# Performance work log

Measured on AMD Instinct MI355X. Metric: run time of the kernel, lower is better.

## Reference

```python
import jax, jax.numpy as jnp
import numpy as np

N_NODES = 50000
N_EDGES = 800000
D = 128  # node_dim == edge_dim
NEG_SLOPE = 0.2


def setup_inputs() -> dict:
    key = jax.random.key(0)
    ks = jax.random.split(key, 16)
    w = lambda k, shp: (jax.random.normal(k, shp, dtype=jnp.float32) * 0.02)
    b = lambda: jnp.zeros((D,), dtype=jnp.float32)
    return {
        "V": jax.random.normal(ks[0], (N_NODES, D), dtype=jnp.float32),
        "E": jax.random.normal(ks[1], (N_EDGES, D), dtype=jnp.float32),
        "src": jax.random.randint(ks[2], (N_EDGES,), 0, N_NODES, dtype=jnp.int32),
        "dst": jax.random.randint(ks[3], (N_EDGES,), 0, N_NODES, dtype=jnp.int32),
        # NodePooling: two node_dim->node_dim linears
        "Wp1": w(ks[4], (D, D)), "bp1": b(),
        "Wp2": w(ks[5], (D, D)), "bp2": b(),
        # GenMessage.A: MLP with nb_mlp_layer=2 linears (edge_dim->edge_dim)
        "WA1": w(ks[6], (D, D)), "bA1": b(),
        "WA2": w(ks[7], (D, D)), "bA2": b(),
        # GenMessage.B (scale) and .C (shift): edge_dim->node_dim
        "WB": w(ks[8], (D, D)), "bB": b(),
        "WC": w(ks[9], (D, D)), "bC": b(),
    }


def reference(V, E, src, dst, Wp1, bp1, Wp2, bp2, WA1, bA1, WA2, bA2, WB, bB, WC, bC):
    lrelu = lambda x: jax.nn.leaky_relu(x, NEG_SLOPE)
    # V = act(V); G.ndata['V'] = pooling(V)
    Vp = lrelu(lrelu(V) @ Wp1.T + bp1) @ Wp2.T + bp2  # [N, D]
    # edge MLP on edge features (ReLU between linears, none after last)
    x = jax.nn.relu(E @ WA1.T + bA1) @ WA2.T + bA2    # [E, D]
    scale = jax.nn.sigmoid(x @ WB.T + bB)             # [E, D]
    shift = x @ WC.T + bC                             # [E, D]
    # per-edge gated message using gathered source node features
    msg = scale * Vp[src] + shift                     # [E, D]
    # scatter-sum into destination nodes (dgl.fn.sum)
    out = jax.ops.segment_sum(msg, dst, num_segments=N_NODES)  # [N, D]
    return out
```

## Files before the change

kernel.cpp:

```cpp
#include <hip/hip_runtime.h>
#include <hip/hip_bf16.h>

typedef __attribute__((ext_vector_type(8))) short bf16x8;
typedef __attribute__((ext_vector_type(4))) float f32x4;

#define DD 128

static __device__ __forceinline__ unsigned short f2bf(float f) {
    __bf16 h = (__bf16)f;
    return __builtin_bit_cast(unsigned short, h);
}
static __device__ __forceinline__ unsigned int pk2bf(float lo, float hi) {
    return ((unsigned int)f2bf(hi) << 16) | (unsigned int)f2bf(lo);
}
static __device__ __forceinline__ float bf2f(unsigned short h) {
    unsigned int u = ((unsigned int)h) << 16;
    return __builtin_bit_cast(float, u);
}

static __device__ __forceinline__ void lds_barrier() {
    asm volatile("s_waitcnt lgkmcnt(0)" ::: "memory");
    __builtin_amdgcn_s_barrier();
    asm volatile("" ::: "memory");
}

__global__ __launch_bounds__(256) void k_convert_hist(
    const float* __restrict__ w0, const float* __restrict__ w1,
    const float* __restrict__ w2, const float* __restrict__ w3,
    const float* __restrict__ w4, const float* __restrict__ w5,
    unsigned short* __restrict__ wbf,
    const int* __restrict__ dst, int* __restrict__ counts, int nE, int use_perm) {
    int i = blockIdx.x * blockDim.x + threadIdx.x;
    if (i < 6 * 16384) {
        int m = i >> 14, k = i & 16383;
        const float* s = (m == 0) ? w0 : (m == 1) ? w1 : (m == 2) ? w2 : (m == 3) ? w3
                         : (m == 4) ? w4 : w5;
        wbf[i] = f2bf(s[k]);
    }
    if (use_perm)
        for (int e = i; e < nE; e += gridDim.x * blockDim.x)
            atomicAdd(&counts[dst[e]], 1);
}

__global__ __launch_bounds__(256) void k_scanA(const int* __restrict__ counts,
                                               int* __restrict__ cursor,
                                               int* __restrict__ partials, int nN) {
    __shared__ int ps[256];
    const int tid = threadIdx.x;
    const int i = blockIdx.x * 256 + tid;
    int v = (i < nN) ? counts[i] : 0;
    ps[tid] = v;
    __syncthreads();
    for (int off = 1; off < 256; off <<= 1) {
        int add = (tid >= off) ? ps[tid - off] : 0;
        __syncthreads();
        ps[tid] += add;
        __syncthreads();
    }
    if (i < nN) cursor[i] = ps[tid] - v;
    if (tid == 255) partials[blockIdx.x] = ps[255];
}

__global__ __launch_bounds__(256) void k_scanB(int* __restrict__ cursor,
                                               const int* __restrict__ partials,
                                               int nN, int nB) {
    __shared__ int ps[256];
    const int tid = threadIdx.x;
    int v = 0;
    for (int j = tid; j < blockIdx.x; j += 256) v += partials[j];
    ps[tid] = v;
    __syncthreads();
    for (int off = 1; off < 256; off <<= 1) {
        int add = (tid >= off) ? ps[tid - off] : 0;
        __syncthreads();
        ps[tid] += add;
        __syncthreads();
    }
    const int offset = ps[255];
    const int i = blockIdx.x * 256 + tid;
    if (i < nN) cursor[i] += offset;
}

__global__ __launch_bounds__(256, 3) void k_nodes(
    const float* __restrict__ V, const unsigned short* __restrict__ wbf,
    const float* __restrict__ bp1, const float* __restrict__ bp2,
    unsigned short* __restrict__ Vp, int nN, int nTiles,
    const int* __restrict__ dst, int* __restrict__ cursor,
    int* __restrict__ perm, int nE, int use_perm)
{
    if (use_perm)
        for (int e = blockIdx.x * blockDim.x + threadIdx.x; e < nE; e += gridDim.x * blockDim.x) {
            int pos = atomicAdd(&cursor[dst[e]], 1);
            perm[pos] = e;
        }

    const int lane = threadIdx.x & 63;
    const int wave = threadIdx.x >> 6;
    const int lr = lane & 15, lg = lane >> 4;

    bf16x8 B1[2][4], B2[2][4];
#pragma unroll
    for (int ct = 0; ct < 2; ++ct)
#pragma unroll
        for (int kk = 0; kk < 4; ++kk) {
            int j = wave * 32 + ct * 16 + lr;
            int k0 = kk * 32 + lg * 8;
            B1[ct][kk] = *(const bf16x8*)(wbf + 0 * 16384 + j * DD + k0);
            B2[ct][kk] = *(const bf16x8*)(wbf + 1 * 16384 + j * DD + k0);
        }
    float b1v[2], b2v[2];
#pragma unroll
    for (int ct = 0; ct < 2; ++ct) {
        int c = wave * 32 + ct * 16 + lr;
        b1v[ct] = bp1[c]; b2v[ct] = bp2[c];
    }
    __shared__ alignas(16) unsigned short xb[32][136];

    for (int t = blockIdx.x; t < nTiles; t += gridDim.x) {
        const int r0 = t * 32;
        bf16x8 A[2][4];
#pragma unroll
        for (int rg = 0; rg < 2; ++rg)
#pragma unroll
            for (int kk = 0; kk < 4; ++kk) {
                int row = r0 + rg * 16 + lr; if (row >= nN) row = nN - 1;
                const float4* p = (const float4*)(V + (size_t)row * DD + kk * 32 + lg * 8);
                float4 f0 = p[0], f1 = p[1];
                float v[8] = {f0.x, f0.y, f0.z, f0.w, f1.x, f1.y, f1.z, f1.w};
                bf16x8 a;
#pragma unroll
                for (int e = 0; e < 8; ++e) {
                    float x = v[e];
                    x = x > 0.f ? x : 0.2f * x;
                    a[e] = (short)f2bf(x);
                }
                A[rg][kk] = a;
            }
#pragma unroll
        for (int rg = 0; rg < 2; ++rg)
#pragma unroll
            for (int ct = 0; ct < 2; ++ct) {
                f32x4 acc = {0.f, 0.f, 0.f, 0.f};
#pragma unroll
                for (int kk = 0; kk < 4; ++kk)
                    acc = __builtin_amdgcn_mfma_f32_16x16x32_bf16(A[rg][kk], B1[ct][kk], acc, 0, 0, 0);
#pragma unroll
                for (int r = 0; r < 4; ++r) {
                    float x = acc[r] + b1v[ct];
                    x = x > 0.f ? x : 0.2f * x;
                    xb[rg * 16 + lg * 4 + r][wave * 32 + ct * 16 + lr] = f2bf(x);
                }
            }
        lds_barrier();
        bf16x8 A2[2][4];
#pragma unroll
        for (int rg = 0; rg < 2; ++rg)
#pragma unroll
            for (int kk = 0; kk < 4; ++kk)
                A2[rg][kk] = *(const bf16x8*)&xb[rg * 16 + lr][kk * 32 + lg * 8];
#pragma unroll
        for (int rg = 0; rg < 2; ++rg)
#pragma unroll
            for (int ct = 0; ct < 2; ++ct) {
                f32x4 acc = {0.f, 0.f, 0.f, 0.f};
#pragma unroll
                for (int kk = 0; kk < 4; ++kk)
                    acc = __builtin_amdgcn_mfma_f32_16x16x32_bf16(A2[rg][kk], B2[ct][kk], acc, 0, 0, 0);
#pragma unroll
                for (int r = 0; r < 4; ++r) {
                    int row = r0 + rg * 16 + lg * 4 + r;
                    if (row < nN)
                        Vp[(size_t)row * DD + wave * 32 + ct * 16 + lr] = f2bf(acc[r] + b2v[ct]);
                }
            }
        lds_barrier();
    }
}

__global__ __launch_bounds__(256, 2) void k_edges(
    const float* __restrict__ E, const int* __restrict__ src, const int* __restrict__ dst,
    const int* __restrict__ perm, int use_perm,
    const unsigned short* __restrict__ wbf,
    const float* __restrict__ bA1, const float* __restrict__ bA2,
    const float* __restrict__ bB, const float* __restrict__ bC,
    const unsigned short* __restrict__ Vp, float* __restrict__ out, int nE, int nTiles)
{
    const int lane = threadIdx.x & 63;
    const int wave = threadIdx.x >> 6;
    const int lr = lane & 15, lg = lane >> 4;
    const int srow = threadIdx.x >> 3;
    const int schunk = threadIdx.x & 7;

    bf16x8 B1[2][4], B2[2][4], B3[2][4], B4[2][4];
#pragma unroll
    for (int ct = 0; ct < 2; ++ct)
#pragma unroll
        for (int kk = 0; kk < 4; ++kk) {
            int j = wave * 32 + ct * 16 + lr;
            int k0 = kk * 32 + lg * 8;
            const unsigned short* p = wbf + 2 * 16384 + j * DD + k0;
            B1[ct][kk] = *(const bf16x8*)(p);
            B2[ct][kk] = *(const bf16x8*)(p + 16384);
            B3[ct][kk] = *(const bf16x8*)(p + 32768);
            B4[ct][kk] = *(const bf16x8*)(p + 49152);
        }
    float b1v[2], b2v[2], b3v[2], b4v[2];
#pragma unroll
    for (int ct = 0; ct < 2; ++ct) {
        int c = wave * 32 + ct * 16 + lr;
        b1v[ct] = bA1[c]; b2v[ct] = bA2[c]; b3v[ct] = bB[c]; b4v[ct] = bC[c];
    }
    __shared__ alignas(16) unsigned short xb[2][32][136];
    __shared__ alignas(16) unsigned short Eb[2][32][136];
    __shared__ alignas(8)  unsigned short gv[32][132];
    __shared__ int dstb[32];

    const int gstep = gridDim.x;
    int t = blockIdx.x;

    auto pidx = [&](int i) -> int {
        if (i >= nE) i = nE - 1;
        return use_perm ? perm[i] : i;
    };

    int pe_t = pidx(t * 32 + srow);
    int pe1  = pidx((t + gstep) * 32 + srow);
    uint2 g0, g1, g2, g3;
    {
        const uint2* vp2 = (const uint2*)(Vp + (size_t)src[pe_t] * DD);
        g0 = vp2[schunk]; g1 = vp2[schunk + 8]; g2 = vp2[schunk + 16]; g3 = vp2[schunk + 24];
    }
    int pd = ((t * 32 + srow) < nE) ? dst[pe_t] : -1;
    float4 pf0, pf1, pf2, pf3;
    {
        const float4* np = (const float4*)(E + (size_t)pe1 * DD + schunk * 16);
        pf0 = np[0]; pf1 = np[1]; pf2 = np[2]; pf3 = np[3];
    }
    {
        const float4* p = (const float4*)(E + (size_t)pe_t * DD + schunk * 16);
        float4 f0 = p[0], f1 = p[1], f2 = p[2], f3 = p[3];
        uint4 w0 = make_uint4(pk2bf(f0.x, f0.y), pk2bf(f0.z, f0.w),
                              pk2bf(f1.x, f1.y), pk2bf(f1.z, f1.w));
        uint4 w1 = make_uint4(pk2bf(f2.x, f2.y), pk2bf(f2.z, f2.w),
                              pk2bf(f3.x, f3.y), pk2bf(f3.z, f3.w));
        uint4* wp = (uint4*)&Eb[0][srow][schunk * 16];
        wp[0] = w0; wp[1] = w1;
    }
    lds_barrier();
    int cur = 0;

    for (; t < nTiles; t += gstep) {
        bf16x8 A[2][4];
#pragma unroll
        for (int rg = 0; rg < 2; ++rg)
#pragma unroll
            for (int kk = 0; kk < 4; ++kk)
                A[rg][kk] = *(const bf16x8*)&Eb[cur][rg * 16 + lr][kk * 32 + lg * 8];
#pragma unroll
        for (int rg = 0; rg < 2; ++rg)
#pragma unroll
            for (int ct = 0; ct < 2; ++ct) {
                f32x4 acc = {0.f, 0.f, 0.f, 0.f};
#pragma unroll
                for (int kk = 0; kk < 4; ++kk)
                    acc = __builtin_amdgcn_mfma_f32_16x16x32_bf16(A[rg][kk], B1[ct][kk], acc, 0, 0, 0);
#pragma unroll
                for (int r = 0; r < 4; ++r) {
                    float x = fmaxf(acc[r] + b1v[ct], 0.f);
                    xb[0][rg * 16 + lg * 4 + r][wave * 32 + ct * 16 + lr] = f2bf(x);
                }
            }
        lds_barrier();
        *(uint2*)&gv[srow][schunk * 4]      = g0;
        *(uint2*)&gv[srow][schunk * 4 + 32] = g1;
        *(uint2*)&gv[srow][schunk * 4 + 64] = g2;
        *(uint2*)&gv[srow][schunk * 4 + 96] = g3;
        if (schunk == 0) dstb[srow] = pd;
        {
            uint4 w0 = make_uint4(pk2bf(pf0.x, pf0.y), pk2bf(pf0.z, pf0.w),
                                  pk2bf(pf1.x, pf1.y), pk2bf(pf1.z, pf1.w));
            uint4 w1 = make_uint4(pk2bf(pf2.x, pf2.y), pk2bf(pf2.z, pf2.w),
                                  pk2bf(pf3.x, pf3.y), pk2bf(pf3.z, pf3.w));
            uint4* wp = (uint4*)&Eb[cur ^ 1][srow][schunk * 16];
            wp[0] = w0; wp[1] = w1;
        }
        int pe2 = pidx((t + 2 * gstep) * 32 + srow);
        float4 nf0, nf1, nf2, nf3;
        {
            const float4* np = (const float4*)(E + (size_t)pe2 * DD + schunk * 16);
            nf0 = np[0]; nf1 = np[1]; nf2 = np[2]; nf3 = np[3];
        }
        {
            int sl = src[pe1];
            const uint2* nvp2 = (const uint2*)(Vp + (size_t)sl * DD);
            g0 = nvp2[schunk]; g1 = nvp2[schunk + 8]; g2 = nvp2[schunk + 16]; g3 = nvp2[schunk + 24];
        }
        int pdn = (((t + gstep) * 32 + srow) < nE) ? dst[pe1] : -1;
        bf16x8 A2[2][4];
#pragma unroll
        for (int rg = 0; rg < 2; ++rg)
#pragma unroll
            for (int kk = 0; kk < 4; ++kk)
                A2[rg][kk] = *(const bf16x8*)&xb[0][rg * 16 + lr][kk * 32 + lg * 8];
#pragma unroll
        for (int rg = 0; rg < 2; ++rg)
#pragma unroll
            for (int ct = 0; ct < 2; ++ct) {
                f32x4 acc = {0.f, 0.f, 0.f, 0.f};
#pragma unroll
                for (int kk = 0; kk < 4; ++kk)
                    acc = __builtin_amdgcn_mfma_f32_16x16x32_bf16(A2[rg][kk], B2[ct][kk], acc, 0, 0, 0);
#pragma unroll
                for (int r = 0; r < 4; ++r)
                    xb[1][rg * 16 + lg * 4 + r][wave * 32 + ct * 16 + lr] = f2bf(acc[r] + b2v[ct]);
            }
        lds_barrier();
        bf16x8 A3[2][4];
#pragma unroll
        for (int rg = 0; rg < 2; ++rg)
#pragma unroll
            for (int kk = 0; kk < 4; ++kk)
                A3[rg][kk] = *(const bf16x8*)&xb[1][rg * 16 + lr][kk * 32 + lg * 8];
        float mA0[4], mA1[4], mB0[4], mB1[4];
#pragma unroll
        for (int rg = 0; rg < 2; ++rg)
#pragma unroll
            for (int ct = 0; ct < 2; ++ct) {
                f32x4 aB = {0.f, 0.f, 0.f, 0.f}, aC = {0.f, 0.f, 0.f, 0.f};
#pragma unroll
                for (int kk = 0; kk < 4; ++kk) {
                    aB = __builtin_amdgcn_mfma_f32_16x16x32_bf16(A3[rg][kk], B3[ct][kk], aB, 0, 0, 0);
                    aC = __builtin_amdgcn_mfma_f32_16x16x32_bf16(A3[rg][kk], B4[ct][kk], aC, 0, 0, 0);
                }
                const int col = wave * 32 + ct * 16 + lr;
#pragma unroll
                for (int r = 0; r < 4; ++r) {
                    float e = __expf(-(aB[r] + b3v[ct]));
                    float sc = __builtin_amdgcn_rcpf(1.f + e);
                    float sh = aC[r] + b4v[ct];
                    float v = bf2f(gv[rg * 16 + lg * 4 + r][col]);
                    float m = sc * v + sh;
                    if (rg == 0) { if (ct == 0) mA0[r] = m; else mA1[r] = m; }
                    else         { if (ct == 0) mB0[r] = m; else mB1[r] = m; }
                }
            }
        {
            const int col0 = wave * 32 + lr;
            const int col1 = wave * 32 + 16 + lr;
            int cdA = -1, cdB = -1;
            float cvA0 = 0.f, cvA1 = 0.f, cvB0 = 0.f, cvB1 = 0.f;
#pragma unroll
            for (int s = 0; s < 4; ++s) {
                int   ndA  = __shfl_up(cdA, 16, 64);
                float nvA0 = __shfl_up(cvA0, 16, 64);
                float nvA1 = __shfl_up(cvA1, 16, 64);
                int   ndB  = __shfl_up(cdB, 16, 64);
                float nvB0 = __shfl_up(cvB0, 16, 64);
                float nvB1 = __shfl_up(cvB1, 16, 64);
                if (lg == s) {
                    if (s == 0) { ndA = -2; ndB = -2; }
                    int dA[5], dB[5];
#pragma unroll
                    for (int r = 0; r < 4; ++r) {
                        dA[r] = dstb[s * 4 + r];
                        dB[r] = dstb[16 + s * 4 + r];
                    }
                    dA[4] = (s < 3) ? dstb[s * 4 + 4]      : -2147483647;
                    dB[4] = (s < 3) ? dstb[16 + s * 4 + 4] : -2147483647;
                    float a0 = (ndA == dA[0]) ? nvA0 : 0.f;
                    float a1 = (ndA == dA[0]) ? nvA1 : 0.f;
#pragma unroll
                    for (int r = 0; r < 4; ++r) {
                        a0 += mA0[r]; a1 += mA1[r];
                        if (dA[r + 1] != dA[r]) {
                            if (dA[r] >= 0) {
                                unsafeAtomicAdd(out + (size_t)dA[r] * DD + col0, a0);
                                unsafeAtomicAdd(out + (size_t)dA[r] * DD + col1, a1);
                            }
                            a0 = 0.f; a1 = 0.f;
                        }
                    }
                    cdA = (dA[4] == dA[3]) ? dA[3] : -2;
                    cvA0 = a0; cvA1 = a1;
                    float b0 = (ndB == dB[0]) ? nvB0 : 0.f;
                    float b1 = (ndB == dB[0]) ? nvB1 : 0.f;
#pragma unroll
                    for (int r = 0; r < 4; ++r) {
                        b0 += mB0[r]; b1 += mB1[r];
                        if (dB[r + 1] != dB[r]) {
                            if (dB[r] >= 0) {
                                unsafeAtomicAdd(out + (size_t)dB[r] * DD + col0, b0);
                                unsafeAtomicAdd(out + (size_t)dB[r] * DD + col1, b1);
                            }
                            b0 = 0.f; b1 = 0.f;
                        }
                    }
                    cdB = (dB[4] == dB[3]) ? dB[3] : -2;
                    cvB0 = b0; cvB1 = b1;
                }
            }
        }
        cur ^= 1;
        pf0 = nf0; pf1 = nf1; pf2 = nf2; pf3 = nf3;
        pe1 = pe2; pd = pdn;
    }
}

extern "C" void kernel_launch(void* const* d_in, const int* in_sizes, int n_in,
                              void* d_out, int out_size, void* d_ws, size_t ws_size,
                              hipStream_t stream) {
    const float* V   = (const float*)d_in[0];
    const float* E   = (const float*)d_in[1];
    const int*   src = (const int*)d_in[2];
    const int*   dst = (const int*)d_in[3];
    const float* Wp1 = (const float*)d_in[4];  const float* bp1 = (const float*)d_in[5];
    const float* Wp2 = (const float*)d_in[6];  const float* bp2 = (const float*)d_in[7];
    const float* WA1 = (const float*)d_in[8];  const float* bA1 = (const float*)d_in[9];
    const float* WA2 = (const float*)d_in[10]; const float* bA2 = (const float*)d_in[11];
    const float* WB  = (const float*)d_in[12]; const float* bB  = (const float*)d_in[13];
    const float* WC  = (const float*)d_in[14]; const float* bC  = (const float*)d_in[15];
    float* out = (float*)d_out;

    const int nN = in_sizes[0] / DD;
    const int nE = in_sizes[1] / DD;
    const int nTilesN = (nN + 31) / 32;
    const int nTilesE = (nE + 31) / 32;
    const int nB = (nN + 255) / 256;

    char* wsb = (char*)d_ws;
    unsigned short* wbf = (unsigned short*)wsb;
    unsigned short* Vp  = (unsigned short*)(wsb + 196608);
    size_t off_counts = 196608 + (size_t)nN * 256;
    int* counts   = (int*)(wsb + off_counts);
    int* cursor   = (int*)(wsb + off_counts + (size_t)nN * 4);
    int* perm     = (int*)(wsb + off_counts + (size_t)nN * 8);
    int* partials = (int*)(wsb + off_counts + (size_t)nN * 8 + (size_t)nE * 4);
    size_t ws_need = off_counts + (size_t)nN * 8 + (size_t)nE * 4 + (size_t)nB * 4;
    int use_perm = (ws_size >= ws_need) ? 1 : 0;

    hipMemsetAsync(d_out, 0, (size_t)out_size * sizeof(float), stream);
    if (use_perm) hipMemsetAsync(counts, 0, (size_t)nN * 4, stream);

    k_convert_hist<<<1024, 256, 0, stream>>>(Wp1, Wp2, WA1, WA2, WB, WC, wbf,
                                             dst, counts, nE, use_perm);
    if (use_perm) {
        k_scanA<<<nB, 256, 0, stream>>>(counts, cursor, partials, nN);
        k_scanB<<<nB, 256, 0, stream>>>(cursor, partials, nN, nB);
    }

    int gN = nTilesN < 768 ? nTilesN : 768;
    k_nodes<<<gN, 256, 0, stream>>>(V, wbf, bp1, bp2, Vp, nN, nTilesN,
                                    dst, cursor, perm, nE, use_perm);
    int gE = nTilesE < 512 ? nTilesE : 512;
    k_edges<<<gE, 256, 0, stream>>>(E, src, dst, perm, use_perm, wbf,
                                    bA1, bA2, bB, bC, Vp, out, nE, nTilesE);
}
```

Measured before the change: 353.0 us.

## Stage messages in per-wave LDS and segment-reduce them per column before atomics

The edge kernel's epilogue previously combined results across lane groups with a four-step shuffle chain before issuing atomics. Now each wave writes its 32x32 message tile to a per-wave LDS buffer and reduces runs of equal destinations serially: each lane owns one column and half of the rows, and flushes one atomic per run. The change also adjusts LDS row padding and raises wave priority around the MFMA loops. This trades shuffles and divergent branches for extra LDS traffic. It can also issue more atomics, because runs are split at the 16-row halves.

```diff
diff --git a/kernel.cpp b/kernel.cpp
--- a/kernel.cpp
+++ b/kernel.cpp
@@ -22,6 +22,9 @@
     asm volatile("s_waitcnt lgkmcnt(0)" ::: "memory");
     __builtin_amdgcn_s_barrier();
     asm volatile("" ::: "memory");
+}
+static __device__ __forceinline__ void lds_fence() {
+    asm volatile("s_waitcnt lgkmcnt(0)" ::: "memory");
 }
 
 __global__ __launch_bounds__(256) void k_convert_hist(
@@ -114,7 +117,7 @@
         int c = wave * 32 + ct * 16 + lr;
         b1v[ct] = bp1[c]; b2v[ct] = bp2[c];
     }
-    __shared__ alignas(16) unsigned short xb[32][136];
+    __shared__ alignas(16) unsigned short xb[32][132];
 
     for (int t = blockIdx.x; t < nTiles; t += gridDim.x) {
         const int r0 = t * 32;
@@ -210,9 +213,10 @@
         int c = wave * 32 + ct * 16 + lr;
         b1v[ct] = bA1[c]; b2v[ct] = bA2[c]; b3v[ct] = bB[c]; b4v[ct] = bC[c];
     }
-    __shared__ alignas(16) unsigned short xb[2][32][136];
-    __shared__ alignas(16) unsigned short Eb[2][32][136];
-    __shared__ alignas(8)  unsigned short gv[32][132];
+    __shared__ alignas(16) unsigned short xb[2][32][132];
+    __shared__ alignas(16) unsigned short Eb[2][32][132];
+    __shared__ alignas(8)  unsigned short gv[32][140];
+    __shared__ alignas(16) float msgw[4][32][34];
     __shared__ int dstb[32];
 
     const int gstep = gridDim.x;
@@ -261,9 +265,11 @@
 #pragma unroll
             for (int ct = 0; ct < 2; ++ct) {
                 f32x4 acc = {0.f, 0.f, 0.f, 0.f};
+                __builtin_amdgcn_s_setprio(1);
 #pragma unroll
                 for (int kk = 0; kk < 4; ++kk)
                     acc = __builtin_amdgcn_mfma_f32_16x16x32_bf16(A[rg][kk], B1[ct][kk], acc, 0, 0, 0);
+                __builtin_amdgcn_s_setprio(0);
 #pragma unroll
                 for (int r = 0; r < 4; ++r) {
                     float x = fmaxf(acc[r] + b1v[ct], 0.f);
@@ -307,9 +313,11 @@
 #pragma unroll
             for (int ct = 0; ct < 2; ++ct) {
                 f32x4 acc = {0.f, 0.f, 0.f, 0.f};
+                __builtin_amdgcn_s_setprio(1);
 #pragma unroll
                 for (int kk = 0; kk < 4; ++kk)
                     acc = __builtin_amdgcn_mfma_f32_16x16x32_bf16(A2[rg][kk], B2[ct][kk], acc, 0, 0, 0);
+                __builtin_amdgcn_s_setprio(0);
 #pragma unroll
                 for (int r = 0; r < 4; ++r)
                     xb[1][rg * 16 + lg * 4 + r][wave * 32 + ct * 16 + lr] = f2bf(acc[r] + b2v[ct]);
@@ -321,82 +329,44 @@
 #pragma unroll
             for (int kk = 0; kk < 4; ++kk)
                 A3[rg][kk] = *(const bf16x8*)&xb[1][rg * 16 + lr][kk * 32 + lg * 8];
-        float mA0[4], mA1[4], mB0[4], mB1[4];
 #pragma unroll
         for (int rg = 0; rg < 2; ++rg)
 #pragma unroll
             for (int ct = 0; ct < 2; ++ct) {
                 f32x4 aB = {0.f, 0.f, 0.f, 0.f}, aC = {0.f, 0.f, 0.f, 0.f};
+                __builtin_amdgcn_s_setprio(1);
 #pragma unroll
                 for (int kk = 0; kk < 4; ++kk) {
                     aB = __builtin_amdgcn_mfma_f32_16x16x32_bf16(A3[rg][kk], B3[ct][kk], aB, 0, 0, 0);
                     aC = __builtin_amdgcn_mfma_f32_16x16x32_bf16(A3[rg][kk], B4[ct][kk], aC, 0, 0, 0);
                 }
-                const int col = wave * 32 + ct * 16 + lr;
+                __builtin_amdgcn_s_setprio(0);
 #pragma unroll
                 for (int r = 0; r < 4; ++r) {
                     float e = __expf(-(aB[r] + b3v[ct]));
                     float sc = __builtin_amdgcn_rcpf(1.f + e);
                     float sh = aC[r] + b4v[ct];
-                    float v = bf2f(gv[rg * 16 + lg * 4 + r][col]);
-                    float m = sc * v + sh;
-                    if (rg == 0) { if (ct == 0) mA0[r] = m; else mA1[r] = m; }
-                    else         { if (ct == 0) mB0[r] = m; else mB1[r] = m; }
-                }
-            }
+                    float v = bf2f(gv[rg * 16 + lg * 4 + r][wave * 32 + ct * 16 + lr]);
+                    msgw[wave][rg * 16 + lg * 4 + r][ct * 16 + lr] = sc * v + sh;
+                }
+            }
+        lds_fence();
         {
-            const int col0 = wave * 32 + lr;
-            const int col1 = wave * 32 + 16 + lr;
-            int cdA = -1, cdB = -1;
-            float cvA0 = 0.f, cvA1 = 0.f, cvB0 = 0.f, cvB1 = 0.f;
-#pragma unroll
-            for (int s = 0; s < 4; ++s) {
-                int   ndA  = __shfl_up(cdA, 16, 64);
-                float nvA0 = __shfl_up(cvA0, 16, 64);
-                float nvA1 = __shfl_up(cvA1, 16, 64);
-                int   ndB  = __shfl_up(cdB, 16, 64);
-                float nvB0 = __shfl_up(cvB0, 16, 64);
-                float nvB1 = __shfl_up(cvB1, 16, 64);
-                if (lg == s) {
-                    if (s == 0) { ndA = -2; ndB = -2; }
-                    int dA[5], dB[5];
-#pragma unroll
-                    for (int r = 0; r < 4; ++r) {
-                        dA[r] = dstb[s * 4 + r];
-                        dB[r] = dstb[16 + s * 4 + r];
-                    }
-                    dA[4] = (s < 3) ? dstb[s * 4 + 4]      : -2147483647;
-                    dB[4] = (s < 3) ? dstb[16 + s * 4 + 4] : -2147483647;
-                    float a0 = (ndA == dA[0]) ? nvA0 : 0.f;
-                    float a1 = (ndA == dA[0]) ? nvA1 : 0.f;
-#pragma unroll
-                    for (int r = 0; r < 4; ++r) {
-                        a0 += mA0[r]; a1 += mA1[r];
-                        if (dA[r + 1] != dA[r]) {
-                            if (dA[r] >= 0) {
-                                unsafeAtomicAdd(out + (size_t)dA[r] * DD + col0, a0);
-                                unsafeAtomicAdd(out + (size_t)dA[r] * DD + col1, a1);
-                            }
-                            a0 = 0.f; a1 = 0.f;
-                        }
-                    }
-                    cdA = (dA[4] == dA[3]) ? dA[3] : -2;
-                    cvA0 = a0; cvA1 = a1;
-                    float b0 = (ndB == dB[0]) ? nvB0 : 0.f;
-                    float b1 = (ndB == dB[0]) ? nvB1 : 0.f;
-#pragma unroll
-                    for (int r = 0; r < 4; ++r) {
-                        b0 += mB0[r]; b1 += mB1[r];
-                        if (dB[r + 1] != dB[r]) {
-                            if (dB[r] >= 0) {
-                                unsafeAtomicAdd(out + (size_t)dB[r] * DD + col0, b0);
-                                unsafeAtomicAdd(out + (size_t)dB[r] * DD + col1, b1);
-                            }
-                            b0 = 0.f; b1 = 0.f;
-                        }
-                    }
-                    cdB = (dB[4] == dB[3]) ? dB[3] : -2;
-                    cvB0 = b0; cvB1 = b1;
+            const int cw = lane & 31;
+            const int half = lane >> 5;
+            const int col = wave * 32 + cw;
+            const int rbase = half * 16;
+            float acc = 0.f;
+#pragma unroll
+            for (int rr = 0; rr < 16; ++rr) {
+                const int rrow = rbase + rr;
+                acc += msgw[wave][rrow][cw];
+                int d = dstb[rrow];
+                bool flush = (rr == 15) || (dstb[rrow + 1] != d);
+                if (flush) {
+                    if (d >= 0)
+                        unsafeAtomicAdd(out + (size_t)d * DD + col, acc);
+                    acc = 0.f;
                 }
             }
         }
```

Result: no change. 348.8 us (-1.2%).

## Stream edge weights from cache per tile and raise edge-kernel occupancy

Applied to the files above, without the earlier changes.

The edge kernel stops holding all four 128x128 bf16 weight fragments in registers. It reloads them per column tile from global memory (L1/L2 resident), which allows launch bounds of 3 blocks per CU and a larger grid. The scatter pass also writes src/dst sorted alongside perm, so the edge loop reads them contiguously instead of through an indirect load. Other changes: the E staging buffer goes from double to single buffering, LDS padding is adjusted, and s_setprio wraps the MFMA chains. In exchange, each tile issues more weight loads, and the single E buffer could add a read/write hazard across the barriers.

```diff
diff --git a/kernel.cpp b/kernel.cpp
--- a/kernel.cpp
+++ b/kernel.cpp
@@ -85,13 +85,17 @@
     const float* __restrict__ V, const unsigned short* __restrict__ wbf,
     const float* __restrict__ bp1, const float* __restrict__ bp2,
     unsigned short* __restrict__ Vp, int nN, int nTiles,
-    const int* __restrict__ dst, int* __restrict__ cursor,
-    int* __restrict__ perm, int nE, int use_perm)
+    const int* __restrict__ src, const int* __restrict__ dst,
+    int* __restrict__ cursor, int* __restrict__ perm,
+    int* __restrict__ srcS, int* __restrict__ dstS, int nE, int use_perm)
 {
     if (use_perm)
         for (int e = blockIdx.x * blockDim.x + threadIdx.x; e < nE; e += gridDim.x * blockDim.x) {
-            int pos = atomicAdd(&cursor[dst[e]], 1);
+            int d = dst[e];
+            int pos = atomicAdd(&cursor[d], 1);
             perm[pos] = e;
+            srcS[pos] = src[e];
+            dstS[pos] = d;
         }
 
     const int lane = threadIdx.x & 63;
@@ -114,7 +118,7 @@
         int c = wave * 32 + ct * 16 + lr;
         b1v[ct] = bp1[c]; b2v[ct] = bp2[c];
     }
-    __shared__ alignas(16) unsigned short xb[32][136];
+    __shared__ alignas(16) unsigned short xb[32][132];
 
     for (int t = blockIdx.x; t < nTiles; t += gridDim.x) {
         const int r0 = t * 32;
@@ -177,9 +181,10 @@
     }
 }
 
-__global__ __launch_bounds__(256, 2) void k_edges(
+__global__ __launch_bounds__(256, 3) void k_edges(
     const float* __restrict__ E, const int* __restrict__ src, const int* __restrict__ dst,
-    const int* __restrict__ perm, int use_perm,
+    const int* __restrict__ perm, const int* __restrict__ srcS, const int* __restrict__ dstS,
+    int use_perm,
     const unsigned short* __restrict__ wbf,
     const float* __restrict__ bA1, const float* __restrict__ bA2,
     const float* __restrict__ bB, const float* __restrict__ bC,
@@ -191,49 +196,41 @@
     const int srow = threadIdx.x >> 3;
     const int schunk = threadIdx.x & 7;
 
-    bf16x8 B1[2][4], B2[2][4], B3[2][4], B4[2][4];
-#pragma unroll
-    for (int ct = 0; ct < 2; ++ct)
-#pragma unroll
-        for (int kk = 0; kk < 4; ++kk) {
-            int j = wave * 32 + ct * 16 + lr;
-            int k0 = kk * 32 + lg * 8;
-            const unsigned short* p = wbf + 2 * 16384 + j * DD + k0;
-            B1[ct][kk] = *(const bf16x8*)(p);
-            B2[ct][kk] = *(const bf16x8*)(p + 16384);
-            B3[ct][kk] = *(const bf16x8*)(p + 32768);
-            B4[ct][kk] = *(const bf16x8*)(p + 49152);
-        }
+    const unsigned short* wBase = wbf + 2 * 16384 + (wave * 32 + lr) * DD + lg * 8;
+
     float b1v[2], b2v[2], b3v[2], b4v[2];
 #pragma unroll
     for (int ct = 0; ct < 2; ++ct) {
         int c = wave * 32 + ct * 16 + lr;
         b1v[ct] = bA1[c]; b2v[ct] = bA2[c]; b3v[ct] = bB[c]; b4v[ct] = bC[c];
     }
-    __shared__ alignas(16) unsigned short xb[2][32][136];
-    __shared__ alignas(16) unsigned short Eb[2][32][136];
-    __shared__ alignas(8)  unsigned short gv[32][132];
+    __shared__ alignas(16) unsigned short xb[2][32][132];
+    __shared__ alignas(16) unsigned short Eb[32][132];
+    __shared__ alignas(8)  unsigned short gv[32][140];
     __shared__ int dstb[32];
 
     const int gstep = gridDim.x;
     int t = blockIdx.x;
 
-    auto pidx = [&](int i) -> int {
-        if (i >= nE) i = nE - 1;
-        return use_perm ? perm[i] : i;
+    auto loadMeta = [&](int i, int& pe, int& sl, int& pd) {
+        bool valid = (i < nE); if (!valid) i = nE - 1;
+        if (use_perm) { pe = perm[i]; sl = srcS[i]; pd = dstS[i]; }
+        else          { pe = i;       sl = src[i];  pd = dst[i];  }
+        if (!valid) pd = -1;
     };
 
-    int pe_t = pidx(t * 32 + srow);
-    int pe1  = pidx((t + gstep) * 32 + srow);
+    int pe_t, sl_t, pd;
+    loadMeta(t * 32 + srow, pe_t, sl_t, pd);
+    int peN, slN, pdN;
+    loadMeta((t + gstep) * 32 + srow, peN, slN, pdN);
     uint2 g0, g1, g2, g3;
     {
-        const uint2* vp2 = (const uint2*)(Vp + (size_t)src[pe_t] * DD);
+        const uint2* vp2 = (const uint2*)(Vp + (size_t)sl_t * DD);
         g0 = vp2[schunk]; g1 = vp2[schunk + 8]; g2 = vp2[schunk + 16]; g3 = vp2[schunk + 24];
     }
-    int pd = ((t * 32 + srow) < nE) ? dst[pe_t] : -1;
     float4 pf0, pf1, pf2, pf3;
     {
-        const float4* np = (const float4*)(E + (size_t)pe1 * DD + schunk * 16);
+        const float4* np = (const float4*)(E + (size_t)peN * DD + schunk * 16);
         pf0 = np[0]; pf1 = np[1]; pf2 = np[2]; pf3 = np[3];
     }
     {
@@ -243,11 +240,10 @@
                               pk2bf(f1.x, f1.y), pk2bf(f1.z, f1.w));
         uint4 w1 = make_uint4(pk2bf(f2.x, f2.y), pk2bf(f2.z, f2.w),
                               pk2bf(f3.x, f3.y), pk2bf(f3.z, f3.w));
-        uint4* wp = (uint4*)&Eb[0][srow][schunk * 16];
+        uint4* wp = (uint4*)&Eb[srow][schunk * 16];
         wp[0] = w0; wp[1] = w1;
     }
     lds_barrier();
-    int cur = 0;
 
     for (; t < nTiles; t += gstep) {
         bf16x8 A[2][4];
@@ -255,21 +251,28 @@
         for (int rg = 0; rg < 2; ++rg)
 #pragma unroll
             for (int kk = 0; kk < 4; ++kk)
-                A[rg][kk] = *(const bf16x8*)&Eb[cur][rg * 16 + lr][kk * 32 + lg * 8];
-#pragma unroll
-        for (int rg = 0; rg < 2; ++rg)
-#pragma unroll
-            for (int ct = 0; ct < 2; ++ct) {
+                A[rg][kk] = *(const bf16x8*)&Eb[rg * 16 + lr][kk * 32 + lg * 8];
+#pragma unroll
+        for (int ct = 0; ct < 2; ++ct) {
+            bf16x8 Bt[4];
+#pragma unroll
+            for (int kk = 0; kk < 4; ++kk)
+                Bt[kk] = *(const bf16x8*)(wBase + 0 * 16384 + ct * 16 * DD + kk * 32);
+#pragma unroll
+            for (int rg = 0; rg < 2; ++rg) {
                 f32x4 acc = {0.f, 0.f, 0.f, 0.f};
+                __builtin_amdgcn_s_setprio(1);
 #pragma unroll
                 for (int kk = 0; kk < 4; ++kk)
-                    acc = __builtin_amdgcn_mfma_f32_16x16x32_bf16(A[rg][kk], B1[ct][kk], acc, 0, 0, 0);
+                    acc = __builtin_amdgcn_mfma_f32_16x16x32_bf16(A[rg][kk], Bt[kk], acc, 0, 0, 0);
+                __builtin_amdgcn_s_setprio(0);
 #pragma unroll
                 for (int r = 0; r < 4; ++r) {
                     float x = fmaxf(acc[r] + b1v[ct], 0.f);
                     xb[0][rg * 16 + lg * 4 + r][wave * 32 + ct * 16 + lr] = f2bf(x);
                 }
             }
+        }
         lds_barrier();
         *(uint2*)&gv[srow][schunk * 4]      = g0;
         *(uint2*)&gv[srow][schunk * 4 + 32] = g1;
@@ -281,21 +284,20 @@
                                   pk2bf(pf1.x, pf1.y), pk2bf(pf1.z, pf1.w));
             uint4 w1 = make_uint4(pk2bf(pf2.x, pf2.y), pk2bf(pf2.z, pf2.w),
                                   pk2bf(pf3.x, pf3.y), pk2bf(pf3.z, pf3.w));
-            uint4* wp = (uint4*)&Eb[cur ^ 1][srow][schunk * 16];
+            uint4* wp = (uint4*)&Eb[srow][schunk * 16];
             wp[0] = w0; wp[1] = w1;
         }
-        int pe2 = pidx((t + 2 * gstep) * 32 + srow);
+        int pe2, sl2, pd2;
+        loadMeta((t + 2 * gstep) * 32 + srow, pe2, sl2, pd2);
         float4 nf0, nf1, nf2, nf3;
         {
             const float4* np = (const float4*)(E + (size_t)pe2 * DD + schunk * 16);
             nf0 = np[0]; nf1 = np[1]; nf2 = np[2]; nf3 = np[3];
         }
         {
-            int sl = src[pe1];
-            const uint2* nvp2 = (const uint2*)(Vp + (size_t)sl * DD);
+            const uint2* nvp2 = (const uint2*)(Vp + (size_t)slN * DD);
             g0 = nvp2[schunk]; g1 = nvp2[schunk + 8]; g2 = nvp2[schunk + 16]; g3 = nvp2[schunk + 24];
         }
-        int pdn = (((t + gstep) * 32 + srow) < nE) ? dst[pe1] : -1;
         bf16x8 A2[2][4];
 #pragma unroll
         for (int rg = 0; rg < 2; ++rg)
@@ -303,17 +305,24 @@
             for (int kk = 0; kk < 4; ++kk)
                 A2[rg][kk] = *(const bf16x8*)&xb[0][rg * 16 + lr][kk * 32 + lg * 8];
 #pragma unroll
-        for (int rg = 0; rg < 2; ++rg)
-#pragma unroll
-            for (int ct = 0; ct < 2; ++ct) {
+        for (int ct = 0; ct < 2; ++ct) {
+            bf16x8 Bt[4];
+#pragma unroll
+            for (int kk = 0; kk < 4; ++kk)
+                Bt[kk] = *(const bf16x8*)(wBase + 1 * 16384 + ct * 16 * DD + kk * 32);
+#pragma unroll
+            for (int rg = 0; rg < 2; ++rg) {
                 f32x4 acc = {0.f, 0.f, 0.f, 0.f};
+                __builtin_amdgcn_s_setprio(1);
 #pragma unroll
                 for (int kk = 0; kk < 4; ++kk)
-                    acc = __builtin_amdgcn_mfma_f32_16x16x32_bf16(A2[rg][kk], B2[ct][kk], acc, 0, 0, 0);
+                    acc = __builtin_amdgcn_mfma_f32_16x16x32_bf16(A2[rg][kk], Bt[kk], acc, 0, 0, 0);
+                __builtin_amdgcn_s_setprio(0);
 #pragma unroll
                 for (int r = 0; r < 4; ++r)
                     xb[1][rg * 16 + lg * 4 + r][wave * 32 + ct * 16 + lr] = f2bf(acc[r] + b2v[ct]);
             }
+        }
         lds_barrier();
         bf16x8 A3[2][4];
 #pragma unroll
@@ -323,15 +332,23 @@
                 A3[rg][kk] = *(const bf16x8*)&xb[1][rg * 16 + lr][kk * 32 + lg * 8];
         float mA0[4], mA1[4], mB0[4], mB1[4];
 #pragma unroll
-        for (int rg = 0; rg < 2; ++rg)
-#pragma unroll
-            for (int ct = 0; ct < 2; ++ct) {
+        for (int ct = 0; ct < 2; ++ct) {
+            bf16x8 B3t[4], B4t[4];
+#pragma unroll
+            for (int kk = 0; kk < 4; ++kk) {
+                B3t[kk] = *(const bf16x8*)(wBase + 2 * 16384 + ct * 16 * DD + kk * 32);
+                B4t[kk] = *(const bf16x8*)(wBase + 3 * 16384 + ct * 16 * DD + kk * 32);
+            }
+#pragma unroll
+            for (int rg = 0; rg < 2; ++rg) {
                 f32x4 aB = {0.f, 0.f, 0.f, 0.f}, aC = {0.f, 0.f, 0.f, 0.f};
+                __builtin_amdgcn_s_setprio(1);
 #pragma unroll
                 for (int kk = 0; kk < 4; ++kk) {
-                    aB = __builtin_amdgcn_mfma_f32_16x16x32_bf16(A3[rg][kk], B3[ct][kk], aB, 0, 0, 0);
-                    aC = __builtin_amdgcn_mfma_f32_16x16x32_bf16(A3[rg][kk], B4[ct][kk], aC, 0, 0, 0);
-                }
+                    aB = __builtin_amdgcn_mfma_f32_16x16x32_bf16(A3[rg][kk], B3t[kk], aB, 0, 0, 0);
+                    aC = __builtin_amdgcn_mfma_f32_16x16x32_bf16(A3[rg][kk], B4t[kk], aC, 0, 0, 0);
+                }
+                __builtin_amdgcn_s_setprio(0);
                 const int col = wave * 32 + ct * 16 + lr;
 #pragma unroll
                 for (int r = 0; r < 4; ++r) {
@@ -344,6 +361,7 @@
                     else         { if (ct == 0) mB0[r] = m; else mB1[r] = m; }
                 }
             }
+        }
         {
             const int col0 = wave * 32 + lr;
             const int col1 = wave * 32 + 16 + lr;
@@ -400,9 +418,8 @@
                 }
             }
         }
-        cur ^= 1;
         pf0 = nf0; pf1 = nf1; pf2 = nf2; pf3 = nf3;
-        pe1 = pe2; pd = pdn;
+        pd = pdN; pdN = pd2; slN = sl2;
     }
 }
 
@@ -430,13 +447,14 @@
     char* wsb = (char*)d_ws;
     unsigned short* wbf = (unsigned short*)wsb;
     unsigned short* Vp  = (unsigned short*)(wsb + 196608);
-    size_t off_counts = 196608 + (size_t)nN * 256;
-    int* counts   = (int*)(wsb + off_counts);
-    int* cursor   = (int*)(wsb + off_counts + (size_t)nN * 4);
-    int* perm     = (int*)(wsb + off_counts + (size_t)nN * 8);
-    int* partials = (int*)(wsb + off_counts + (size_t)nN * 8 + (size_t)nE * 4);
-    size_t ws_need = off_counts + (size_t)nN * 8 + (size_t)nE * 4 + (size_t)nB * 4;
-    int use_perm = (ws_size >= ws_need) ? 1 : 0;
+    size_t off = 196608 + (size_t)nN * 256;
+    int* counts   = (int*)(wsb + off); off += (size_t)nN * 4;
+    int* cursor   = (int*)(wsb + off); off += (size_t)nN * 4;
+    int* perm     = (int*)(wsb + off); off += (size_t)nE * 4;
+    int* srcS     = (int*)(wsb + off); off += (size_t)nE * 4;
+    int* dstS     = (int*)(wsb + off); off += (size_t)nE * 4;
+    int* partials = (int*)(wsb + off); off += (size_t)nB * 4;
+    int use_perm = (ws_size >= off) ? 1 : 0;
 
     hipMemsetAsync(d_out, 0, (size_t)out_size * sizeof(float), stream);
     if (use_perm) hipMemsetAsync(counts, 0, (size_t)nN * 4, stream);
@@ -450,8 +468,8 @@
 
     int gN = nTilesN < 768 ? nTilesN : 768;
     k_nodes<<<gN, 256, 0, stream>>>(V, wbf, bp1, bp2, Vp, nN, nTilesN,
-                                    dst, cursor, perm, nE, use_perm);
-    int gE = nTilesE < 512 ? nTilesE : 512;
-    k_edges<<<gE, 256, 0, stream>>>(E, src, dst, perm, use_perm, wbf,
+                                    src, dst, cursor, perm, srcS, dstS, nE, use_perm);
+    int gE = nTilesE < 768 ? nTilesE : 768;
+    k_edges<<<gE, 256, 0, stream>>>(E, src, dst, perm, srcS, dstS, use_perm, wbf,
                                     bA1, bA2, bB, bC, Vp, out, nE, nTilesE);
 }
```

Result: slower. 726.6 us (+105.9%).
